# Optimization experiments

Hardware: AMD Instinct MI355X
Metric: run time of the kernel (lower is better)

## Reference

```python
import jax, jax.numpy as jnp
import numpy as np

TOPK = 2
SCALE = 32.0 / 16.0  # alpha / rank
EPS = 1e-20


def setup_inputs() -> dict:
    key = jax.random.key(0)
    ks = jax.random.split(key, 6)
    B, S, D = 4, 4096, 2048
    E, R, QO, VO = 8, 16, 2048, 2048
    return {
        "hidden_states": jax.random.normal(ks[0], (B, S, D), dtype=jnp.float32),
        "router_weight": jax.random.normal(ks[1], (E, D), dtype=jnp.float32) * 0.02,
        "q_lora_a": jax.random.normal(ks[2], (E, D, R), dtype=jnp.float32) * 0.02,
        "q_lora_b": jax.random.normal(ks[3], (E, R, QO), dtype=jnp.float32) * 0.02,
        "v_lora_a": jax.random.normal(ks[4], (E, D, R), dtype=jnp.float32) * 0.02,
        "v_lora_b": jax.random.normal(ks[5], (E, R, VO), dtype=jnp.float32) * 0.02,
    }


def reference(hidden_states, router_weight, q_lora_a, q_lora_b, v_lora_a, v_lora_b):
    orig_shape = hidden_states.shape[:-1]
    D = hidden_states.shape[-1]
    E = router_weight.shape[0]
    h = hidden_states.reshape(-1, D)                       # [T, D]

    # --- routing ---
    logits = h @ router_weight.T                           # [T, E]
    probs = jax.nn.softmax(logits, axis=-1)
    scores, idx = jax.lax.top_k(probs, TOPK)               # [T, K]
    scores = scores / (jnp.sum(scores, axis=-1, keepdims=True) + EPS)
    # dense per-expert combine weight (0 for unselected experts), incl. LoRA scale
    w = jnp.sum(jax.nn.one_hot(idx, E, dtype=h.dtype) * scores[..., None], axis=1) * SCALE  # [T, E]

    # --- grouped LoRA (dense over experts; E and rank are small) ---
    q_low = jnp.einsum('td,edr->ter', h, q_lora_a) * w[:, :, None]  # [T, E, R]
    v_low = jnp.einsum('td,edr->ter', h, v_lora_a) * w[:, :, None]
    q_delta = jnp.einsum('ter,erq->tq', q_low, q_lora_b)            # [T, QO]
    v_delta = jnp.einsum('ter,erv->tv', v_low, v_lora_b)            # [T, VO]

    return (q_delta.reshape(*orig_shape, q_delta.shape[-1]),
            v_delta.reshape(*orig_shape, v_delta.shape[-1]))
```

## Files before the change

kernel.cpp:

```cpp
#include <hip/hip_runtime.h>

#define T_TOKENS 16384
#define DIM 2048
#define NE 8
#define QOUT 2048
#define LSCALE 2.0f

typedef __attribute__((ext_vector_type(4))) float f32x4;
typedef __attribute__((ext_vector_type(8))) short s16x8;
typedef __attribute__((ext_vector_type(4))) short s16x4;

__device__ __forceinline__ short f2bf(float f) {
  unsigned u = __builtin_bit_cast(unsigned, f);
  u += 0x7fffu + ((u >> 16) & 1u);
  return (short)(u >> 16);
}

__device__ __forceinline__ void barrier_lds() {
  asm volatile("s_waitcnt lgkmcnt(0)" ::: "memory");
  __builtin_amdgcn_s_barrier();
}

__global__ __launch_bounds__(256) void k_pack(
    const float* __restrict__ qa, const float* __restrict__ qb,
    const float* __restrict__ va, const float* __restrict__ vb,
    short* __restrict__ Bq1, short* __restrict__ Bv1,
    short* __restrict__ Bq2, short* __restrict__ Bv2) {
  int tid = blockIdx.x * 256 + threadIdx.x;
  if (tid < 65536) {
    int mat = tid >> 15;
    int idx = tid & 32767;
    int d8 = idx >> 7, c = idx & 127;
    int e = c >> 4, r = c & 15;
    const float* src = mat ? va : qa;
    short* dst = mat ? Bv1 : Bq1;
    s16x8 v;
#pragma unroll
    for (int j = 0; j < 8; ++j)
      v[j] = f2bf(src[((size_t)e * DIM + d8 * 8 + j) * 16 + r]);
    *(s16x8*)(dst + (size_t)idx * 8) = v;
  } else {
    int t2 = tid - 65536;
    int mat = t2 >> 15;
    int idx = t2 & 32767;
    int k8 = idx >> 11, c = idx & 2047;
    const float* src = mat ? vb : qb;
    short* dst = mat ? Bv2 : Bq2;
    s16x8 v;
#pragma unroll
    for (int j = 0; j < 8; ++j)
      v[j] = f2bf(src[(size_t)(k8 * 8 + j) * QOUT + c]);
    *(s16x8*)(dst + (size_t)idx * 8) = v;
  }
}

__global__ __launch_bounds__(512) void k_fused(
    const float* __restrict__ h, const float* __restrict__ rw,
    const short* __restrict__ Bq1, const short* __restrict__ Bv1,
    const short* __restrict__ Bq2, const short* __restrict__ Bv2,
    float* __restrict__ out) {
  __shared__ short At[2][32][72];
  __shared__ short low[32][264];
  __shared__ float wl[32][NE];

  const int tid = threadIdx.x;
  const int lane = tid & 63, wv = tid >> 6;
  const int lrow = lane & 15, lk = lane >> 4;
  const int row0 = blockIdx.x * 32;
  const int r  = tid >> 4;
  const int kq = (tid & 15) * 4;

  const float* hrow = h + (size_t)(row0 + r) * DIM + kq;
  const short* B1 = (wv >= 4) ? Bv1 : Bq1;
  int cc2[2];
#pragma unroll
  for (int ct = 0; ct < 2; ++ct) cc2[ct] = (wv & 3) * 32 + ct * 16 + lrow;

  float4 hv = *(const float4*)(hrow);

  float lg[NE] = {0.f, 0.f, 0.f, 0.f, 0.f, 0.f, 0.f, 0.f};
  f32x4 acc1[2][2] = {};

#pragma unroll 1
  for (int kb = 0; kb < DIM; kb += 64) {
    const int cur = (kb >> 6) & 1;
    float4 hvn = *(const float4*)(hrow + ((kb + 64) & (DIM - 1)));
    s16x8 bA[2], bB[2];
#pragma unroll
    for (int ct = 0; ct < 2; ++ct) {
      int d8 = (kb >> 3) + lk;
      bA[ct] = *(const s16x8*)(B1 + ((size_t)d8 * 128 + cc2[ct]) * 8);
      bB[ct] = *(const s16x8*)(B1 + ((size_t)(d8 + 4) * 128 + cc2[ct]) * 8);
    }
    s16x4 hb4;
    hb4[0] = f2bf(hv.x); hb4[1] = f2bf(hv.y);
    hb4[2] = f2bf(hv.z); hb4[3] = f2bf(hv.w);
    *(s16x4*)&At[cur][r][kq] = hb4;
#pragma unroll 1
    for (int g = 0; g < 2; ++g) {
#pragma unroll
      for (int e = 0; e < 4; ++e) {
        float4 rv = *(const float4*)(rw + (g * 4 + e) * DIM + kb + kq);
        lg[g * 4 + e] += hv.x * rv.x + hv.y * rv.y + hv.z * rv.z + hv.w * rv.w;
      }
    }
    barrier_lds();
    s16x8 a0[2], a1[2];
#pragma unroll
    for (int rt = 0; rt < 2; ++rt) {
      a0[rt] = *(const s16x8*)&At[cur][rt * 16 + lrow][lk * 8];
      a1[rt] = *(const s16x8*)&At[cur][rt * 16 + lrow][32 + lk * 8];
    }
#pragma unroll
    for (int rt = 0; rt < 2; ++rt)
#pragma unroll
      for (int ct = 0; ct < 2; ++ct) {
        acc1[rt][ct] = __builtin_amdgcn_mfma_f32_16x16x32_bf16(bA[ct], a0[rt], acc1[rt][ct], 0, 0, 0);
        acc1[rt][ct] = __builtin_amdgcn_mfma_f32_16x16x32_bf16(bB[ct], a1[rt], acc1[rt][ct], 0, 0, 0);
      }
    hv = hvn;
  }

#pragma unroll
  for (int e = 0; e < NE; ++e) {
    lg[e] += __shfl_xor(lg[e], 1, 64);
    lg[e] += __shfl_xor(lg[e], 2, 64);
    lg[e] += __shfl_xor(lg[e], 4, 64);
    lg[e] += __shfl_xor(lg[e], 8, 64);
  }
  float mx = lg[0];
#pragma unroll
  for (int e = 1; e < NE; ++e) mx = fmaxf(mx, lg[e]);
  float p[NE], sum = 0.f;
#pragma unroll
  for (int e = 0; e < NE; ++e) { p[e] = expf(lg[e] - mx); sum += p[e]; }
  int i1 = 0; float v1 = p[0];
#pragma unroll
  for (int e = 1; e < NE; ++e) if (p[e] > v1) { v1 = p[e]; i1 = e; }
  float v2 = -1.f; int i2 = 0;
#pragma unroll
  for (int e = 0; e < NE; ++e) if (e != i1 && p[e] > v2) { v2 = p[e]; i2 = e; }
  float s1 = v1 / sum, s2 = v2 / sum;
  float dn = s1 + s2 + 1e-20f;
  float w1 = s1 / dn * LSCALE, w2 = s2 / dn * LSCALE;
  if ((tid & 15) < 8) {
    int el = tid & 7;
    wl[r][el] = (el == i1) ? w1 : ((el == i2) ? w2 : 0.f);
  }
  __syncthreads();

#pragma unroll
  for (int rt = 0; rt < 2; ++rt)
#pragma unroll
    for (int ct = 0; ct < 2; ++ct) {
      int tok = rt * 16 + lrow;
      float wgt = wl[tok][(wv & 3) * 2 + ct];
      s16x4 v;
#pragma unroll
      for (int j = 0; j < 4; ++j) v[j] = f2bf(acc1[rt][ct][j] * wgt);
      *(s16x4*)&low[tok][wv * 32 + ct * 16 + lk * 4] = v;
    }
  barrier_lds();

  const int m = wv >> 2;
  const int cwave = (wv & 3) * 512;
  const short* B2 = m ? Bv2 : Bq2;
  float* op = out + (size_t)m * T_TOKENS * QOUT;

  s16x8 bc[4];
#pragma unroll
  for (int ct = 0; ct < 4; ++ct) {
    int c = cwave + ct * 16 + lrow;
    bc[ct] = *(const s16x8*)(B2 + ((size_t)lk * QOUT + c) * 8);
  }

  f32x4 acc[2][4] = {};
#pragma unroll 4
  for (int it = 0; it < 32; ++it) {
    const int sub = it >> 2, kk = it & 3;
    const int itn = (it + 1) & 31;
    const int subn = itn >> 2, kkn = itn & 3;
    s16x8 bn[4];
#pragma unroll
    for (int ct = 0; ct < 4; ++ct) {
      int c = cwave + subn * 64 + ct * 16 + lrow;
      bn[ct] = *(const s16x8*)(B2 + ((size_t)(kkn * 4 + lk) * QOUT + c) * 8);
    }
    s16x8 a0 = *(const s16x8*)&low[lrow][m * 128 + kk * 32 + lk * 8];
    s16x8 a1 = *(const s16x8*)&low[16 + lrow][m * 128 + kk * 32 + lk * 8];
#pragma unroll
    for (int ct = 0; ct < 4; ++ct) {
      acc[0][ct] = __builtin_amdgcn_mfma_f32_16x16x32_bf16(bc[ct], a0, acc[0][ct], 0, 0, 0);
      acc[1][ct] = __builtin_amdgcn_mfma_f32_16x16x32_bf16(bc[ct], a1, acc[1][ct], 0, 0, 0);
    }
    if (kk == 3) {
      int cb = cwave + sub * 64;
#pragma unroll
      for (int rt = 0; rt < 2; ++rt)
#pragma unroll
        for (int ct = 0; ct < 4; ++ct) {
          int t = row0 + rt * 16 + lrow;
          int col = cb + ct * 16 + lk * 4;
          __builtin_nontemporal_store(acc[rt][ct], (f32x4*)(op + (size_t)t * QOUT + col));
          acc[rt][ct] = (f32x4){0.f, 0.f, 0.f, 0.f};
        }
    }
#pragma unroll
    for (int ct = 0; ct < 4; ++ct) bc[ct] = bn[ct];
  }
}

extern "C" void kernel_launch(void* const* d_in, const int* in_sizes, int n_in,
                              void* d_out, int out_size, void* d_ws, size_t ws_size,
                              hipStream_t stream) {
  const float* h  = (const float*)d_in[0];
  const float* rw = (const float*)d_in[1];
  const float* qa = (const float*)d_in[2];
  const float* qb = (const float*)d_in[3];
  const float* va = (const float*)d_in[4];
  const float* vb = (const float*)d_in[5];
  float* out = (float*)d_out;
  char* ws = (char*)d_ws;

  short* Bq1 = (short*)(ws);
  short* Bv1 = (short*)(ws + (512 << 10));
  short* Bq2 = (short*)(ws + (1024 << 10));
  short* Bv2 = (short*)(ws + (1536 << 10));

  k_pack<<<512, 256, 0, stream>>>(qa, qb, va, vb, Bq1, Bv1, Bq2, Bv2);
  k_fused<<<T_TOKENS / 32, 512, 0, stream>>>(h, rw, Bq1, Bv1, Bq2, Bv2, out);
}
```

Before: 148.6 us.

## Halve token tile to 16 rows with 256-thread blocks and hoist LoRA-B A operands

Each block now handles 16 tokens with 4 waves instead of 32 tokens with 8 waves, which doubles the grid and gives each wave twice the output columns. The low-rank A fragments for the second GEMM are loaded from LDS once into registers before the output loop. The first B2 fragment prefetch is also moved ahead of the barrier. The intent is more blocks for latency hiding and fewer LDS reads, but each wave now reloads B1/B2 weight fragments for half as many tokens, which doubles weight traffic per token.

Result: slower. 180.4 us (+21.4%).

```diff
diff --git a/kernel.cpp b/kernel.cpp
--- a/kernel.cpp
+++ b/kernel.cpp
@@ -54,43 +54,43 @@
   }
 }
 
-__global__ __launch_bounds__(512) void k_fused(
+__global__ __launch_bounds__(256) void k_fused(
     const float* __restrict__ h, const float* __restrict__ rw,
     const short* __restrict__ Bq1, const short* __restrict__ Bv1,
     const short* __restrict__ Bq2, const short* __restrict__ Bv2,
     float* __restrict__ out) {
-  __shared__ short At[2][32][72];
-  __shared__ short low[32][264];
-  __shared__ float wl[32][NE];
+  __shared__ short At[2][16][72];
+  __shared__ short low[16][264];
+  __shared__ float wl[16][NE];
 
   const int tid = threadIdx.x;
   const int lane = tid & 63, wv = tid >> 6;
   const int lrow = lane & 15, lk = lane >> 4;
-  const int row0 = blockIdx.x * 32;
+  const int row0 = blockIdx.x * 16;
   const int r  = tid >> 4;
   const int kq = (tid & 15) * 4;
 
   const float* hrow = h + (size_t)(row0 + r) * DIM + kq;
-  const short* B1 = (wv >= 4) ? Bv1 : Bq1;
-  int cc2[2];
-#pragma unroll
-  for (int ct = 0; ct < 2; ++ct) cc2[ct] = (wv & 3) * 32 + ct * 16 + lrow;
+  const short* B1 = (wv >= 2) ? Bv1 : Bq1;
+  int cc[4];
+#pragma unroll
+  for (int ct = 0; ct < 4; ++ct) cc[ct] = (wv & 1) * 64 + ct * 16 + lrow;
 
   float4 hv = *(const float4*)(hrow);
 
   float lg[NE] = {0.f, 0.f, 0.f, 0.f, 0.f, 0.f, 0.f, 0.f};
-  f32x4 acc1[2][2] = {};
+  f32x4 acc1[4] = {};
 
 #pragma unroll 1
   for (int kb = 0; kb < DIM; kb += 64) {
     const int cur = (kb >> 6) & 1;
     float4 hvn = *(const float4*)(hrow + ((kb + 64) & (DIM - 1)));
-    s16x8 bA[2], bB[2];
-#pragma unroll
-    for (int ct = 0; ct < 2; ++ct) {
+    s16x8 bA[4], bB[4];
+#pragma unroll
+    for (int ct = 0; ct < 4; ++ct) {
       int d8 = (kb >> 3) + lk;
-      bA[ct] = *(const s16x8*)(B1 + ((size_t)d8 * 128 + cc2[ct]) * 8);
-      bB[ct] = *(const s16x8*)(B1 + ((size_t)(d8 + 4) * 128 + cc2[ct]) * 8);
+      bA[ct] = *(const s16x8*)(B1 + ((size_t)d8 * 128 + cc[ct]) * 8);
+      bB[ct] = *(const s16x8*)(B1 + ((size_t)(d8 + 4) * 128 + cc[ct]) * 8);
     }
     s16x4 hb4;
     hb4[0] = f2bf(hv.x); hb4[1] = f2bf(hv.y);
@@ -105,19 +105,13 @@
       }
     }
     barrier_lds();
-    s16x8 a0[2], a1[2];
-#pragma unroll
-    for (int rt = 0; rt < 2; ++rt) {
-      a0[rt] = *(const s16x8*)&At[cur][rt * 16 + lrow][lk * 8];
-      a1[rt] = *(const s16x8*)&At[cur][rt * 16 + lrow][32 + lk * 8];
-    }
-#pragma unroll
-    for (int rt = 0; rt < 2; ++rt)
-#pragma unroll
-      for (int ct = 0; ct < 2; ++ct) {
-        acc1[rt][ct] = __builtin_amdgcn_mfma_f32_16x16x32_bf16(bA[ct], a0[rt], acc1[rt][ct], 0, 0, 0);
-        acc1[rt][ct] = __builtin_amdgcn_mfma_f32_16x16x32_bf16(bB[ct], a1[rt], acc1[rt][ct], 0, 0, 0);
-      }
+    s16x8 a0 = *(const s16x8*)&At[cur][lrow][lk * 8];
+    s16x8 a1 = *(const s16x8*)&At[cur][lrow][32 + lk * 8];
+#pragma unroll
+    for (int ct = 0; ct < 4; ++ct) {
+      acc1[ct] = __builtin_amdgcn_mfma_f32_16x16x32_bf16(bA[ct], a0, acc1[ct], 0, 0, 0);
+      acc1[ct] = __builtin_amdgcn_mfma_f32_16x16x32_bf16(bB[ct], a1, acc1[ct], 0, 0, 0);
+    }
     hv = hvn;
   }
 
@@ -147,26 +141,10 @@
     int el = tid & 7;
     wl[r][el] = (el == i1) ? w1 : ((el == i2) ? w2 : 0.f);
   }
-  __syncthreads();
-
-#pragma unroll
-  for (int rt = 0; rt < 2; ++rt)
-#pragma unroll
-    for (int ct = 0; ct < 2; ++ct) {
-      int tok = rt * 16 + lrow;
-      float wgt = wl[tok][(wv & 3) * 2 + ct];
-      s16x4 v;
-#pragma unroll
-      for (int j = 0; j < 4; ++j) v[j] = f2bf(acc1[rt][ct][j] * wgt);
-      *(s16x4*)&low[tok][wv * 32 + ct * 16 + lk * 4] = v;
-    }
-  barrier_lds();
-
-  const int m = wv >> 2;
-  const int cwave = (wv & 3) * 512;
+
+  const int m = wv >> 1;
+  const int cwave = (wv & 1) * 1024;
   const short* B2 = m ? Bv2 : Bq2;
-  float* op = out + (size_t)m * T_TOKENS * QOUT;
-
   s16x8 bc[4];
 #pragma unroll
   for (int ct = 0; ct < 4; ++ct) {
@@ -174,11 +152,29 @@
     bc[ct] = *(const s16x8*)(B2 + ((size_t)lk * QOUT + c) * 8);
   }
 
-  f32x4 acc[2][4] = {};
+  barrier_lds();
+
+#pragma unroll
+  for (int ct = 0; ct < 4; ++ct) {
+    float wgt = wl[lrow][(wv & 1) * 4 + ct];
+    s16x4 v;
+#pragma unroll
+    for (int j = 0; j < 4; ++j) v[j] = f2bf(acc1[ct][j] * wgt);
+    *(s16x4*)&low[lrow][wv * 64 + ct * 16 + lk * 4] = v;
+  }
+  barrier_lds();
+
+  float* op = out + (size_t)m * T_TOKENS * QOUT;
+  s16x8 a2[4];
+#pragma unroll
+  for (int kk = 0; kk < 4; ++kk)
+    a2[kk] = *(const s16x8*)&low[lrow][m * 128 + kk * 32 + lk * 8];
+
+  f32x4 acc[4] = {};
 #pragma unroll 4
-  for (int it = 0; it < 32; ++it) {
+  for (int it = 0; it < 64; ++it) {
     const int sub = it >> 2, kk = it & 3;
-    const int itn = (it + 1) & 31;
+    const int itn = (it + 1) & 63;
     const int subn = itn >> 2, kkn = itn & 3;
     s16x8 bn[4];
 #pragma unroll
@@ -186,24 +182,18 @@
       int c = cwave + subn * 64 + ct * 16 + lrow;
       bn[ct] = *(const s16x8*)(B2 + ((size_t)(kkn * 4 + lk) * QOUT + c) * 8);
     }
-    s16x8 a0 = *(const s16x8*)&low[lrow][m * 128 + kk * 32 + lk * 8];
-    s16x8 a1 = *(const s16x8*)&low[16 + lrow][m * 128 + kk * 32 + lk * 8];
-#pragma unroll
-    for (int ct = 0; ct < 4; ++ct) {
-      acc[0][ct] = __builtin_amdgcn_mfma_f32_16x16x32_bf16(bc[ct], a0, acc[0][ct], 0, 0, 0);
-      acc[1][ct] = __builtin_amdgcn_mfma_f32_16x16x32_bf16(bc[ct], a1, acc[1][ct], 0, 0, 0);
-    }
+#pragma unroll
+    for (int ct = 0; ct < 4; ++ct)
+      acc[ct] = __builtin_amdgcn_mfma_f32_16x16x32_bf16(bc[ct], a2[kk], acc[ct], 0, 0, 0);
     if (kk == 3) {
       int cb = cwave + sub * 64;
-#pragma unroll
-      for (int rt = 0; rt < 2; ++rt)
-#pragma unroll
-        for (int ct = 0; ct < 4; ++ct) {
-          int t = row0 + rt * 16 + lrow;
-          int col = cb + ct * 16 + lk * 4;
-          __builtin_nontemporal_store(acc[rt][ct], (f32x4*)(op + (size_t)t * QOUT + col));
-          acc[rt][ct] = (f32x4){0.f, 0.f, 0.f, 0.f};
-        }
+      int t = row0 + lrow;
+#pragma unroll
+      for (int ct = 0; ct < 4; ++ct) {
+        int col = cb + ct * 16 + lk * 4;
+        __builtin_nontemporal_store(acc[ct], (f32x4*)(op + (size_t)t * QOUT + col));
+        acc[ct] = (f32x4){0.f, 0.f, 0.f, 0.f};
+      }
     }
 #pragma unroll
     for (int ct = 0; ct < 4; ++ct) bc[ct] = bn[ct];
@@ -228,5 +218,5 @@
   short* Bv2 = (short*)(ws + (1536 << 10));
 
   k_pack<<<512, 256, 0, stream>>>(qa, qb, va, vb, Bq1, Bv1, Bq2, Bv2);
-  k_fused<<<T_TOKENS / 32, 512, 0, stream>>>(h, rw, Bq1, Bv1, Bq2, Bv2, out);
-}
+  k_fused<<<T_TOKENS / 16, 256, 0, stream>>>(h, rw, Bq1, Bv1, Bq2, Bv2, out);
+}
```

## Split q and v projections across a second grid dimension

Applied to the files above, without the earlier changes.

Launches twice as many blocks, one per token tile per projection (q or v), so each block computes only one LoRA path and writes half the output columns per wave group. Each wave now handles one expert column tile in stage one and 256 output columns in stage two, and the stage-two software prefetch of B is replaced by a simpler per-subtile loop. This adds parallelism and shrinks per-block register and LDS use, but each h tile is read twice and the router logits are recomputed in both blocks.

After: 222.6 us. +49.8%, slower.

```diff
diff --git a/kernel.cpp b/kernel.cpp
--- a/kernel.cpp
+++ b/kernel.cpp
@@ -60,38 +60,33 @@
     const short* __restrict__ Bq2, const short* __restrict__ Bv2,
     float* __restrict__ out) {
   __shared__ short At[2][32][72];
-  __shared__ short low[32][264];
+  __shared__ short low[32][136];
   __shared__ float wl[32][NE];
 
   const int tid = threadIdx.x;
   const int lane = tid & 63, wv = tid >> 6;
   const int lrow = lane & 15, lk = lane >> 4;
   const int row0 = blockIdx.x * 32;
+  const int m = blockIdx.y;
   const int r  = tid >> 4;
   const int kq = (tid & 15) * 4;
 
   const float* hrow = h + (size_t)(row0 + r) * DIM + kq;
-  const short* B1 = (wv >= 4) ? Bv1 : Bq1;
-  int cc2[2];
-#pragma unroll
-  for (int ct = 0; ct < 2; ++ct) cc2[ct] = (wv & 3) * 32 + ct * 16 + lrow;
+  const short* B1 = m ? Bv1 : Bq1;
+  const int cc = wv * 16 + lrow;
 
   float4 hv = *(const float4*)(hrow);
 
   float lg[NE] = {0.f, 0.f, 0.f, 0.f, 0.f, 0.f, 0.f, 0.f};
-  f32x4 acc1[2][2] = {};
+  f32x4 acc1[2] = {};
 
 #pragma unroll 1
   for (int kb = 0; kb < DIM; kb += 64) {
     const int cur = (kb >> 6) & 1;
     float4 hvn = *(const float4*)(hrow + ((kb + 64) & (DIM - 1)));
-    s16x8 bA[2], bB[2];
-#pragma unroll
-    for (int ct = 0; ct < 2; ++ct) {
-      int d8 = (kb >> 3) + lk;
-      bA[ct] = *(const s16x8*)(B1 + ((size_t)d8 * 128 + cc2[ct]) * 8);
-      bB[ct] = *(const s16x8*)(B1 + ((size_t)(d8 + 4) * 128 + cc2[ct]) * 8);
-    }
+    const int d8 = (kb >> 3) + lk;
+    s16x8 bA = *(const s16x8*)(B1 + ((size_t)d8 * 128 + cc) * 8);
+    s16x8 bB = *(const s16x8*)(B1 + ((size_t)(d8 + 4) * 128 + cc) * 8);
     s16x4 hb4;
     hb4[0] = f2bf(hv.x); hb4[1] = f2bf(hv.y);
     hb4[2] = f2bf(hv.z); hb4[3] = f2bf(hv.w);
@@ -105,19 +100,13 @@
       }
     }
     barrier_lds();
-    s16x8 a0[2], a1[2];
 #pragma unroll
     for (int rt = 0; rt < 2; ++rt) {
-      a0[rt] = *(const s16x8*)&At[cur][rt * 16 + lrow][lk * 8];
-      a1[rt] = *(const s16x8*)&At[cur][rt * 16 + lrow][32 + lk * 8];
+      s16x8 a0 = *(const s16x8*)&At[cur][rt * 16 + lrow][lk * 8];
+      s16x8 a1 = *(const s16x8*)&At[cur][rt * 16 + lrow][32 + lk * 8];
+      acc1[rt] = __builtin_amdgcn_mfma_f32_16x16x32_bf16(bA, a0, acc1[rt], 0, 0, 0);
+      acc1[rt] = __builtin_amdgcn_mfma_f32_16x16x32_bf16(bB, a1, acc1[rt], 0, 0, 0);
     }
-#pragma unroll
-    for (int rt = 0; rt < 2; ++rt)
-#pragma unroll
-      for (int ct = 0; ct < 2; ++ct) {
-        acc1[rt][ct] = __builtin_amdgcn_mfma_f32_16x16x32_bf16(bA[ct], a0[rt], acc1[rt][ct], 0, 0, 0);
-        acc1[rt][ct] = __builtin_amdgcn_mfma_f32_16x16x32_bf16(bB[ct], a1[rt], acc1[rt][ct], 0, 0, 0);
-      }
     hv = hvn;
   }
 
@@ -147,66 +136,51 @@
     int el = tid & 7;
     wl[r][el] = (el == i1) ? w1 : ((el == i2) ? w2 : 0.f);
   }
-  __syncthreads();
-
-#pragma unroll
-  for (int rt = 0; rt < 2; ++rt)
-#pragma unroll
-    for (int ct = 0; ct < 2; ++ct) {
-      int tok = rt * 16 + lrow;
-      float wgt = wl[tok][(wv & 3) * 2 + ct];
-      s16x4 v;
-#pragma unroll
-      for (int j = 0; j < 4; ++j) v[j] = f2bf(acc1[rt][ct][j] * wgt);
-      *(s16x4*)&low[tok][wv * 32 + ct * 16 + lk * 4] = v;
-    }
   barrier_lds();
 
-  const int m = wv >> 2;
-  const int cwave = (wv & 3) * 512;
+#pragma unroll
+  for (int rt = 0; rt < 2; ++rt) {
+    int tok = rt * 16 + lrow;
+    float wgt = wl[tok][wv];
+    s16x4 v;
+#pragma unroll
+    for (int j = 0; j < 4; ++j) v[j] = f2bf(acc1[rt][j] * wgt);
+    *(s16x4*)&low[tok][wv * 16 + lk * 4] = v;
+  }
+  barrier_lds();
+
   const short* B2 = m ? Bv2 : Bq2;
   float* op = out + (size_t)m * T_TOKENS * QOUT;
-
-  s16x8 bc[4];
-#pragma unroll
-  for (int ct = 0; ct < 4; ++ct) {
-    int c = cwave + ct * 16 + lrow;
-    bc[ct] = *(const s16x8*)(B2 + ((size_t)lk * QOUT + c) * 8);
-  }
-
-  f32x4 acc[2][4] = {};
-#pragma unroll 4
-  for (int it = 0; it < 32; ++it) {
-    const int sub = it >> 2, kk = it & 3;
-    const int itn = (it + 1) & 31;
-    const int subn = itn >> 2, kkn = itn & 3;
-    s16x8 bn[4];
-#pragma unroll
-    for (int ct = 0; ct < 4; ++ct) {
-      int c = cwave + subn * 64 + ct * 16 + lrow;
-      bn[ct] = *(const s16x8*)(B2 + ((size_t)(kkn * 4 + lk) * QOUT + c) * 8);
+  const int cwave = wv * 256;
+
+#pragma unroll 1
+  for (int sub = 0; sub < 4; ++sub) {
+    const int cb = cwave + sub * 64;
+    f32x4 acc[2][4] = {};
+#pragma unroll
+    for (int kk = 0; kk < 4; ++kk) {
+      s16x8 bc[4];
+#pragma unroll
+      for (int ct = 0; ct < 4; ++ct) {
+        int c = cb + ct * 16 + lrow;
+        bc[ct] = *(const s16x8*)(B2 + ((size_t)(kk * 4 + lk) * QOUT + c) * 8);
+      }
+      s16x8 a0 = *(const s16x8*)&low[lrow][kk * 32 + lk * 8];
+      s16x8 a1 = *(const s16x8*)&low[16 + lrow][kk * 32 + lk * 8];
+#pragma unroll
+      for (int ct = 0; ct < 4; ++ct) {
+        acc[0][ct] = __builtin_amdgcn_mfma_f32_16x16x32_bf16(bc[ct], a0, acc[0][ct], 0, 0, 0);
+        acc[1][ct] = __builtin_amdgcn_mfma_f32_16x16x32_bf16(bc[ct], a1, acc[1][ct], 0, 0, 0);
+      }
     }
-    s16x8 a0 = *(const s16x8*)&low[lrow][m * 128 + kk * 32 + lk * 8];
-    s16x8 a1 = *(const s16x8*)&low[16 + lrow][m * 128 + kk * 32 + lk * 8];
-#pragma unroll
-    for (int ct = 0; ct < 4; ++ct) {
-      acc[0][ct] = __builtin_amdgcn_mfma_f32_16x16x32_bf16(bc[ct], a0, acc[0][ct], 0, 0, 0);
-      acc[1][ct] = __builtin_amdgcn_mfma_f32_16x16x32_bf16(bc[ct], a1, acc[1][ct], 0, 0, 0);
-    }
-    if (kk == 3) {
-      int cb = cwave + sub * 64;
-#pragma unroll
-      for (int rt = 0; rt < 2; ++rt)
-#pragma unroll
-        for (int ct = 0; ct < 4; ++ct) {
-          int t = row0 + rt * 16 + lrow;
-          int col = cb + ct * 16 + lk * 4;
-          __builtin_nontemporal_store(acc[rt][ct], (f32x4*)(op + (size_t)t * QOUT + col));
-          acc[rt][ct] = (f32x4){0.f, 0.f, 0.f, 0.f};
-        }
-    }
-#pragma unroll
-    for (int ct = 0; ct < 4; ++ct) bc[ct] = bn[ct];
+#pragma unroll
+    for (int rt = 0; rt < 2; ++rt)
+#pragma unroll
+      for (int ct = 0; ct < 4; ++ct) {
+        int t = row0 + rt * 16 + lrow;
+        int col = cb + ct * 16 + lk * 4;
+        __builtin_nontemporal_store(acc[rt][ct], (f32x4*)(op + (size_t)t * QOUT + col));
+      }
   }
 }
 
@@ -228,5 +202,6 @@
   short* Bv2 = (short*)(ws + (1536 << 10));
 
   k_pack<<<512, 256, 0, stream>>>(qa, qb, va, vb, Bq1, Bv1, Bq2, Bv2);
-  k_fused<<<T_TOKENS / 32, 512, 0, stream>>>(h, rw, Bq1, Bv1, Bq2, Bv2, out);
-}
+  dim3 gf(T_TOKENS / 32, 2);
+  k_fused<<<gf, 512, 0, stream>>>(h, rw, Bq1, Bv1, Bq2, Bv2, out);
+}
```
